# Performance work log

Measured on AMD Instinct MI355X. Metric: run time of the kernel, lower is better.

## Reference

```python
import jax, jax.numpy as jnp
import numpy as np

ALPHA = 0.1  # init kwarg alpha


def setup_inputs() -> dict:
    key = jax.random.key(0)
    k1, k2 = jax.random.split(key)
    x = jax.random.normal(k1, (32, 192, 64, 64), dtype=jnp.float32)
    delta = jax.random.normal(k2, (32, 1, 64, 64), dtype=jnp.float32)
    return {"x_bchw": x, "delta": delta}


def reference(x_bchw, delta):
    # Faithful fixed-shape version of LayerTokenPrune.forward.
    # Kept tokens are stream-compacted to the front (stable, preserving
    # original token order, matching torch.where index order); dropped
    # positions are zero-padded, matching the zero-pad in the original.
    B, C, H, W = x_bchw.shape
    L = H * W
    tok = jnp.transpose(x_bchw, (0, 2, 3, 1)).reshape(B, L, C)  # [B, L, C]

    delta_tok = delta.reshape(B, -1)  # 4-dim delta branch -> [B, L]
    imp = jnp.abs(delta_tok)
    lo = imp.min(axis=1, keepdims=True)
    hi = imp.max(axis=1, keepdims=True)
    rng = jnp.maximum(hi - lo, 1e-3)  # clamp_min(0.001)
    imp = (imp - lo) / rng

    mu = imp.mean(axis=1, keepdims=True)
    sigma = imp.std(axis=1, keepdims=True, ddof=1)  # torch std is unbiased
    theta = mu - ALPHA * sigma
    keep = imp >= theta  # [B, L] bool; max-imp token always kept (theta<=mu<=1)

    # Stable compaction: kept token indices first, in original order.
    # jnp.argsort is stable, so sorting the key (0 for keep, 1 for drop)
    # reproduces torch.where's ascending-index order for kept tokens.
    order = jnp.argsort(jnp.logical_not(keep).astype(jnp.int32), axis=1)  # [B, L]
    gathered = jnp.take_along_axis(tok, order[:, :, None], axis=1)  # [B, L, C]

    counts = keep.sum(axis=1)  # [B]
    valid = (jnp.arange(L)[None, :] < counts[:, None]).astype(tok.dtype)  # [B, L]
    tok_new = gathered * valid[:, :, None]  # zero out pad positions

    # Fixed-shape analogue of the sqrt reshape: pad to full L = H*W grid.
    y = tok_new.reshape(B, H, W, C).transpose(0, 3, 1, 2)  # [B, C, H, W]

    keep_ratio = counts.astype(jnp.float32).mean() / L
    theta_mean = theta.mean()
    return y, keep_ratio, theta_mean
```

## Files before the change

kernel.cpp:

```cpp
#include <hip/hip_runtime.h>
#include <hip/hip_bf16.h>
#include <math.h>

#define B_ 32
#define C_ 192
#define H_ 64
#define W_ 64
#define L_ 4096
#define L4_ 1024
#define NTHREADS 256
#define PER_THREAD 16

__global__ __launch_bounds__(NTHREADS) void stats_scan_kernel(
    const float* __restrict__ delta,
    int*  __restrict__ src_idx,
    int*  __restrict__ counts,
    float* __restrict__ thetas)
{
  const int b = blockIdx.x;
  const int t = threadIdx.x;
  const int lane = t & 63;
  const int wid  = t >> 6;

  __shared__ float  smin[4], smax[4];
  __shared__ float  s_lo, s_rng, s_theta;
  __shared__ double dsum[4], dsum2[4];
  __shared__ int    wsum[4];

  const float* dp = delta + (size_t)b * L_;

  float a[PER_THREAD];
  const float4* d4 = (const float4*)dp;
  #pragma unroll
  for (int i = 0; i < 4; ++i) {
    float4 v = d4[t * 4 + i];
    a[i*4+0] = fabsf(v.x); a[i*4+1] = fabsf(v.y);
    a[i*4+2] = fabsf(v.z); a[i*4+3] = fabsf(v.w);
  }

  float lmin = a[0], lmax = a[0];
  #pragma unroll
  for (int i = 1; i < PER_THREAD; ++i) {
    lmin = fminf(lmin, a[i]);
    lmax = fmaxf(lmax, a[i]);
  }
  #pragma unroll
  for (int off = 32; off; off >>= 1) {
    lmin = fminf(lmin, __shfl_down(lmin, off, 64));
    lmax = fmaxf(lmax, __shfl_down(lmax, off, 64));
  }
  if (lane == 0) { smin[wid] = lmin; smax[wid] = lmax; }
  __syncthreads();
  if (t == 0) {
    float lo = fminf(fminf(smin[0], smin[1]), fminf(smin[2], smin[3]));
    float hi = fmaxf(fmaxf(smax[0], smax[1]), fmaxf(smax[2], smax[3]));
    s_lo  = lo;
    s_rng = fmaxf(hi - lo, 1e-3f);
  }
  __syncthreads();
  const float lo  = s_lo;
  const float rng = s_rng;

  double s = 0.0, s2 = 0.0;
  #pragma unroll
  for (int i = 0; i < PER_THREAD; ++i) {
    float imp = (a[i] - lo) / rng;
    a[i] = imp;
    s  += (double)imp;
    s2 += (double)imp * (double)imp;
  }
  #pragma unroll
  for (int off = 32; off; off >>= 1) {
    s  += __shfl_down(s,  off, 64);
    s2 += __shfl_down(s2, off, 64);
  }
  if (lane == 0) { dsum[wid] = s; dsum2[wid] = s2; }
  __syncthreads();
  if (t == 0) {
    double S  = dsum[0]  + dsum[1]  + dsum[2]  + dsum[3];
    double S2 = dsum2[0] + dsum2[1] + dsum2[2] + dsum2[3];
    double mu  = S / (double)L_;
    double var = (S2 - S * S / (double)L_) / (double)(L_ - 1);
    if (var < 0.0) var = 0.0;
    double sigma = sqrt(var);
    s_theta = (float)(mu - 0.1 * sigma);
  }
  __syncthreads();
  const float theta = s_theta;

  int flags = 0, cnt = 0;
  #pragma unroll
  for (int i = 0; i < PER_THREAD; ++i) {
    int k = (a[i] >= theta) ? 1 : 0;
    cnt += k;
    flags |= (k << i);
  }
  int inc = cnt;
  #pragma unroll
  for (int off = 1; off < 64; off <<= 1) {
    int y = __shfl_up(inc, off, 64);
    if (lane >= off) inc += y;
  }
  if (lane == 63) wsum[wid] = inc;
  __syncthreads();
  int base = inc - cnt;
  #pragma unroll
  for (int w = 0; w < 4; ++w)
    if (w < wid) base += wsum[w];

  int* sb = src_idx + (size_t)b * L_;
  int p = base;
  #pragma unroll
  for (int i = 0; i < PER_THREAD; ++i) {
    if ((flags >> i) & 1) { sb[p++] = t * PER_THREAD + i; }
  }
  if (t == NTHREADS - 1) {
    counts[b] = base + cnt;
    thetas[b] = theta;
  }
}

__global__ __launch_bounds__(64) void finalize_kernel(
    const int* __restrict__ counts, const float* __restrict__ thetas,
    float* __restrict__ out_tail)
{
  const int t = threadIdx.x;
  float c  = (t < B_) ? (float)counts[t] : 0.0f;
  float th = (t < B_) ? thetas[t]        : 0.0f;
  #pragma unroll
  for (int off = 32; off; off >>= 1) {
    c  += __shfl_down(c,  off, 64);
    th += __shfl_down(th, off, 64);
  }
  if (t == 0) {
    out_tail[0] = (c / (float)B_) / (float)L_;
    out_tail[1] = th / (float)B_;
  }
}

__global__ __launch_bounds__(NTHREADS) void gather_kernel(
    const float* __restrict__ x,
    const int*  __restrict__ src_idx,
    const int*  __restrict__ counts,
    float* __restrict__ out)
{
  const int g  = blockIdx.x * NTHREADS + threadIdx.x;
  const int j  = g & (L4_ - 1);
  const int bc = g >> 10;
  const int b  = bc / C_;

  const int  cnt = counts[b];
  const int4 s4  = ((const int4*)(src_idx + (size_t)b * L_))[j];
  const float* xb = x + (size_t)bc * L_;
  const int d0 = j * 4;

  float4 r;
  r.x = (d0 + 0 < cnt) ? xb[s4.x] : 0.0f;
  r.y = (d0 + 1 < cnt) ? xb[s4.y] : 0.0f;
  r.z = (d0 + 2 < cnt) ? xb[s4.z] : 0.0f;
  r.w = (d0 + 3 < cnt) ? xb[s4.w] : 0.0f;
  ((float4*)out)[g] = r;
}

extern "C" void kernel_launch(void* const* d_in, const int* in_sizes, int n_in,
                              void* d_out, int out_size, void* d_ws, size_t ws_size,
                              hipStream_t stream) {
  const float* x     = (const float*)d_in[0];
  const float* delta = (const float*)d_in[1];
  float* out = (float*)d_out;

  int*   src_idx = (int*)d_ws;
  int*   counts  = (int*)((char*)d_ws + (size_t)B_ * L_ * 4);
  float* thetas  = (float*)((char*)d_ws + (size_t)B_ * L_ * 4 + 128);

  const size_t y_elems = (size_t)B_ * C_ * L_;

  stats_scan_kernel<<<B_, NTHREADS, 0, stream>>>(delta, src_idx, counts, thetas);
  finalize_kernel<<<1, 64, 0, stream>>>(counts, thetas, out + y_elems);
  gather_kernel<<<(int)(y_elems / 4 / NTHREADS), NTHREADS, 0, stream>>>(
      x, src_idx, counts, out);
}
```

Baseline: 209.4 us.

## Stage each channel row in LDS and gather from shared memory

```diff
diff --git a/kernel.cpp b/kernel.cpp
--- a/kernel.cpp
+++ b/kernel.cpp
@@ -10,6 +10,8 @@
 #define L4_ 1024
 #define NTHREADS 256
 #define PER_THREAD 16
+
+typedef float  f32x4 __attribute__((ext_vector_type(4)));
 
 __global__ __launch_bounds__(NTHREADS) void stats_scan_kernel(
     const float* __restrict__ delta,
@@ -144,22 +146,37 @@
     const int*  __restrict__ counts,
     float* __restrict__ out)
 {
-  const int g  = blockIdx.x * NTHREADS + threadIdx.x;
-  const int j  = g & (L4_ - 1);
-  const int bc = g >> 10;
+  __shared__ float row[L_];
+
+  const int bc = blockIdx.x;
   const int b  = bc / C_;
+  const int t  = threadIdx.x;
+
+  const float4* x4 = (const float4*)(x + (size_t)bc * L_);
+  float4* r4 = (float4*)row;
+
+  #pragma unroll
+  for (int i = 0; i < 4; ++i) {
+    r4[t + NTHREADS * i] = x4[t + NTHREADS * i];
+  }
+  __syncthreads();
 
   const int  cnt = counts[b];
-  const int4 s4  = ((const int4*)(src_idx + (size_t)b * L_))[j];
-  const float* xb = x + (size_t)bc * L_;
-  const int d0 = j * 4;
+  const int4* s4b = (const int4*)(src_idx + (size_t)b * L_);
+  f32x4* o4 = (f32x4*)(out + (size_t)bc * L_);
 
-  float4 r;
-  r.x = (d0 + 0 < cnt) ? xb[s4.x] : 0.0f;
-  r.y = (d0 + 1 < cnt) ? xb[s4.y] : 0.0f;
-  r.z = (d0 + 2 < cnt) ? xb[s4.z] : 0.0f;
-  r.w = (d0 + 3 < cnt) ? xb[s4.w] : 0.0f;
-  ((float4*)out)[g] = r;
+  #pragma unroll
+  for (int i = 0; i < 4; ++i) {
+    const int j  = t + NTHREADS * i;
+    const int d0 = j * 4;
+    const int4 s = s4b[j];
+    f32x4 r;
+    r.x = (d0 + 0 < cnt) ? row[s.x] : 0.0f;
+    r.y = (d0 + 1 < cnt) ? row[s.y] : 0.0f;
+    r.z = (d0 + 2 < cnt) ? row[s.z] : 0.0f;
+    r.w = (d0 + 3 < cnt) ? row[s.w] : 0.0f;
+    __builtin_nontemporal_store(r, o4 + j);
+  }
 }
 
 extern "C" void kernel_launch(void* const* d_in, const int* in_sizes, int n_in,
@@ -177,6 +194,5 @@
 
   stats_scan_kernel<<<B_, NTHREADS, 0, stream>>>(delta, src_idx, counts, thetas);
   finalize_kernel<<<1, 64, 0, stream>>>(counts, thetas, out + y_elems);
-  gather_kernel<<<(int)(y_elems / 4 / NTHREADS), NTHREADS, 0, stream>>>(
-      x, src_idx, counts, out);
+  gather_kernel<<<B_ * C_, NTHREADS, 0, stream>>>(x, src_idx, counts, out);
 }
```

New measurement: 184.1 us. -12.1%, faster.
